# Kernel optimization log

Measured on AMD Instinct MI355X. Metric: run time of the kernel, lower is better.

The kernel has to match this reference:

```python
import jax, jax.numpy as jnp
import numpy as np
import math

B, S, E, H = 2, 1024, 1024, 8
HD = E // H
M, W, K, GH, R, MR = 128, 32, 8, 128, 8, 8
ATTN_ALPHA, GATE_TEMP, CONTENT_MIX = 3.0, 1.0, 0.25
FFN_H = 4 * E


def _layernorm(z, g, b):
    mu = jnp.mean(z, axis=-1, keepdims=True)
    var = jnp.var(z, axis=-1, keepdims=True)
    return (z - mu) * jax.lax.rsqrt(var + 1e-5) * g + b


def _topk_sparse(logits, k, temp):
    # faithful to torch topk_sparse_weights: hard + (soft - hard).detach()
    soft = jax.nn.softmax(logits / max(temp, 1e-6), axis=-1)
    idx = jax.lax.top_k(soft, k)[1]
    hard = jax.nn.one_hot(idx, logits.shape[-1], dtype=soft.dtype).sum(axis=-2)
    hard = hard / (hard.sum(axis=-1, keepdims=True) + 1e-8)
    return hard + jax.lax.stop_gradient(soft - hard)


def _pos_and_window():
    rel = jnp.arange(-(S - 1), S, dtype=jnp.float32)  # [2S-1]
    p1 = rel / S
    p2 = jnp.sign(rel) * jnp.sqrt(jnp.abs(rel) + 1e-6) / math.sqrt(S)
    pos_kern = jnp.stack([p1, p2], axis=-1)  # [2S-1, 2]
    d = jnp.arange(S, dtype=jnp.float32)
    sigma = S / 4.0
    win = jnp.exp(-(d ** 2) / (2.0 * sigma ** 2))  # [S]
    return pos_kern, win


def setup_inputs() -> dict:
    key = jax.random.key(0)
    ks = jax.random.split(key, 20)
    rn = lambda i, shape, s: jax.random.normal(ks[i], shape, dtype=jnp.float32) * s
    scale = 1.0 / math.sqrt(HD)
    return {
        'x': rn(0, (B, S, E), 1.0),
        'v_w': rn(1, (E, E), 0.02), 'v_b': jnp.zeros((E,), jnp.float32),
        'out_w': rn(2, (E, E), 0.02), 'out_b': jnp.zeros((E,), jnp.float32),
        'qmod_w': rn(3, (E, H), 0.02), 'qmod_b': jnp.zeros((H,), jnp.float32),
        'kmod_w': rn(4, (E, H), 0.02), 'kmod_b': jnp.zeros((H,), jnp.float32),
        'gate_w1': rn(5, (H, E, GH), 0.02), 'gate_b1': jnp.zeros((H, GH), jnp.float32),
        'gate_w2': rn(6, (H, GH, M), 0.02), 'gate_b2': jnp.zeros((H, M), jnp.float32),
        'mod_w1': rn(7, (H, E, GH), 0.02), 'mod_b1': jnp.zeros((H, GH), jnp.float32),
        'mod_w2': rn(8, (H, GH, MR), 0.02), 'mod_b2': jnp.zeros((H, MR), jnp.float32),
        'mod_basis': rn(9, (H, MR, M), 0.05),
        'freqs': rn(10, (H, M, W, 2), 1.5),
        'amps': rn(11, (H, M, W), 0.02) + 0.5,
        'phases': rn(12, (H, M, W), math.pi),
        'content_wq': rn(13, (H, HD, R), scale),
        'content_wk': rn(14, (H, HD, R), scale),
        'ffn_w1': rn(15, (E, FFN_H), 0.02), 'ffn_b1': jnp.zeros((FFN_H,), jnp.float32),
        'ffn_w2': rn(16, (FFN_H, E), 0.02), 'ffn_b2': jnp.zeros((E,), jnp.float32),
        'ln_attn_g': jnp.ones((E,), jnp.float32), 'ln_attn_b': jnp.zeros((E,), jnp.float32),
        'ln_ffn_g': jnp.ones((E,), jnp.float32), 'ln_ffn_b': jnp.zeros((E,), jnp.float32),
    }


def reference(x, v_w, v_b, out_w, out_b, qmod_w, qmod_b, kmod_w, kmod_b,
              gate_w1, gate_b1, gate_w2, gate_b2, mod_w1, mod_b1, mod_w2, mod_b2,
              mod_basis, freqs, amps, phases, content_wq, content_wk,
              ffn_w1, ffn_b1, ffn_w2, ffn_b2, ln_attn_g, ln_attn_b, ln_ffn_g, ln_ffn_b):
    pos_kern, win = _pos_and_window()
    # --- per-sequence gating over mask library (top-k sparse routing) ---
    pooled = x.mean(axis=1)  # [B,E]
    gh = jax.nn.relu(jnp.einsum('be,heg->bhg', pooled, gate_w1) + gate_b1)
    glog = jnp.einsum('bhg,hgm->bhm', gh, gate_w2) + gate_b2  # [B,H,M]
    wsel = _topk_sparse(glog, K, GATE_TEMP)
    mh = jax.nn.relu(jnp.einsum('be,heg->bhg', pooled, mod_w1) + mod_b1)
    mr = jnp.einsum('bhg,hgr->bhr', mh, mod_w2) + mod_b2  # [B,H,MR]
    mod = jnp.einsum('bhr,hrm->bhm', mr, mod_basis)
    wmod = wsel * (1.0 + mod)  # [B,H,M]
    # --- wave-interference synthesis of relative-position kernels ---
    dots = jnp.einsum('ld,hmwd->hmwl', pos_kern, freqs)  # [H,M,W,2S-1]
    waves = jnp.sin(2.0 * math.pi * dots + phases[..., None]) * amps[..., None]
    kernels = waves.sum(axis=2)  # [H,M,2S-1]
    kern = jnp.einsum('bhm,hml->bhl', wmod, kernels)  # [B,H,2S-1]
    # --- Toeplitz gather into causal score matrix ---
    i = jnp.arange(S)
    rel_idx = (i[None, :] - i[:, None]) + (S - 1)  # index of rel = j - i
    scores = kern[:, :, rel_idx]  # [B,H,S,S]
    dist = jnp.clip(i[:, None] - i[None, :], 0, S - 1)
    scores = scores * win[dist]
    qs = x @ qmod_w + qmod_b  # [B,S,H]
    km = x @ kmod_w + kmod_b
    logits = ATTN_ALPHA * scores + qs.transpose(0, 2, 1)[..., None] + km.transpose(0, 2, 1)[:, :, None, :]
    # --- low-rank content term ---
    xh = x.reshape(B, S, H, HD)
    qc = jnp.einsum('bshd,hdr->bhsr', xh, content_wq)
    kc = jnp.einsum('bshd,hdr->bhsr', xh, content_wk)
    logits = logits + CONTENT_MIX * jnp.einsum('bhsr,bhtr->bhst', qc, kc)
    causal = i[:, None] >= i[None, :]
    logits = jnp.where(causal, logits, -jnp.inf)
    attn = jax.nn.softmax(logits, axis=-1)
    v = (x @ v_w + v_b).reshape(B, S, H, HD)
    o = jnp.einsum('bhst,bthd->bshd', attn, v).reshape(B, S, E)
    o = o @ out_w + out_b
    y = _layernorm(x + o, ln_attn_g, ln_attn_b)
    f = jax.nn.gelu(y @ ffn_w1 + ffn_b1) @ ffn_w2 + ffn_b2
    return _layernorm(y + f, ln_ffn_g, ln_ffn_b)
```

## Files before the change

### kernel.cpp

```cpp
#include <hip/hip_runtime.h>
#include <math.h>
#include <stdint.h>

namespace {

constexpr int B_ = 2, S_ = 1024, E_ = 1024, H_ = 8, HD_ = 128;
constexpr int M_ = 128, W_ = 32, GH_ = 128, R_ = 8, MR_ = 8, FFNH_ = 4096;
constexpr int SCH = 32;
constexpr int SPC = S_ / SCH;

typedef __bf16 bf16;
typedef _Float16 f16;
typedef __attribute__((ext_vector_type(8))) __bf16 bf16x8;
typedef __attribute__((ext_vector_type(4))) __bf16 bf16x4;
typedef __attribute__((ext_vector_type(4))) _Float16 f16x4;
typedef __attribute__((ext_vector_type(4))) float f32x4;

__device__ inline float gelu_tanh(float u) {
  float u3 = u * u * u;
  return 0.5f * u * (1.f + tanhf(0.7978845608028654f * (u + 0.044715f * u3)));
}

__device__ __forceinline__ void gl_lds16(const void* g, void* l) {
  __builtin_amdgcn_global_load_lds((const __attribute__((address_space(1))) void*)g,
                                   (__attribute__((address_space(3))) void*)l, 16, 0, 0);
}

template <int NB>
__device__ __forceinline__ void gemm_body(
    const bf16* __restrict__ A, const bf16* __restrict__ BT,
    f16* __restrict__ P, int N, int K, int Kslice, size_t strideB, size_t mn,
    int lin, int gx, int gy, bf16* Asb, bf16* Bsb) {
  int t = threadIdx.x;
  int by = lin % gy;
  int rem = lin / gy;
  int bx = rem % gx;
  int z = rem / gx;
  int bb = z % NB;
  int k0 = (z / NB) * Kslice;
  const bf16* Bbase = BT + (size_t)bb * strideB;
  int row0 = by * 128, col0 = bx * 128;
  int lane = t & 63, wid = t >> 6;
  int wr = wid >> 1, wc = wid & 1;

  const bf16* AgP[4];
  const bf16* BgP[4];
  int ldo[4];
#pragma unroll
  for (int j = 0; j < 4; ++j) {
    int p = t + j * 256;
    int sub = p >> 9;
    int pp = p & 511;
    int rt = ((pp >> 6) << 4) | (pp & 15);
    int kb = (pp >> 4) & 3;
    AgP[j] = A + (size_t)(row0 + rt) * K + k0 + sub * 32 + kb * 8;
    BgP[j] = Bbase + (size_t)(col0 + rt) * K + k0 + sub * 32 + kb * 8;
    ldo[j] = sub * 4096 + pp * 8;
  }

  f32x4 acc[4][4];
#pragma unroll
  for (int m = 0; m < 4; ++m)
#pragma unroll
    for (int n = 0; n < 4; ++n) acc[m][n] = (f32x4){0.f, 0.f, 0.f, 0.f};

#pragma unroll
  for (int j = 0; j < 4; ++j) {
    gl_lds16(AgP[j], &Asb[ldo[j]]);
    gl_lds16(BgP[j], &Bsb[ldo[j]]);
  }

  const int nt = Kslice >> 6;
  for (int kt = 0; kt < nt; ++kt) {
    int cur = kt & 1;
    __syncthreads();
    if (kt + 1 < nt) {
      size_t go = (size_t)(kt + 1) * 64;
      int nb = cur ^ 1;
#pragma unroll
      for (int j = 0; j < 4; ++j) {
        gl_lds16(AgP[j] + go, &Asb[nb * 8192 + ldo[j]]);
        gl_lds16(BgP[j] + go, &Bsb[nb * 8192 + ldo[j]]);
      }
    }
#pragma unroll
    for (int kk = 0; kk < 2; ++kk) {
      bf16x8 af[4], bfr[4];
#pragma unroll
      for (int m = 0; m < 4; ++m)
        af[m] = *(const bf16x8*)&Asb[cur * 8192 + kk * 4096 + ((wr * 4 + m) * 64 + lane) * 8];
#pragma unroll
      for (int n = 0; n < 4; ++n)
        bfr[n] = *(const bf16x8*)&Bsb[cur * 8192 + kk * 4096 + ((wc * 4 + n) * 64 + lane) * 8];
#pragma unroll
      for (int m = 0; m < 4; ++m)
#pragma unroll
        for (int n = 0; n < 4; ++n)
          acc[m][n] = __builtin_amdgcn_mfma_f32_16x16x32_bf16(af[m], bfr[n], acc[m][n], 0, 0, 0);
    }
  }

  f16* Pz = P + (size_t)z * mn;
  int r0 = row0 + wr * 64, c0 = col0 + wc * 64;
#pragma unroll
  for (int m = 0; m < 4; ++m)
#pragma unroll
    for (int n = 0; n < 4; ++n) {
      int col = c0 + n * 16 + (lane & 15);
#pragma unroll
      for (int reg = 0; reg < 4; ++reg) {
        int row = r0 + m * 16 + ((lane >> 4) << 2) + reg;
        Pz[(size_t)row * N + col] = (f16)acc[m][n][reg];
      }
    }
}

__device__ __forceinline__ void wt_tile(const float* __restrict__ w,
                                        bf16* __restrict__ wT, int K, int N,
                                        int bx, int by, float (*tile)[33]) {
  int t = threadIdx.x;
  int n0 = bx * 32, k0 = by * 32;
  int tx = t & 31, ty = t >> 5;
  for (int r = ty; r < 32; r += 8) tile[r][tx] = w[(size_t)(k0 + r) * N + n0 + tx];
  __syncthreads();
  for (int r = ty; r < 32; r += 8) wT[(size_t)(n0 + r) * K + k0 + tx] = (bf16)tile[tx][r];
}

__global__ __launch_bounds__(256) void k_prep(
    const float* __restrict__ x, bf16* __restrict__ xb,
    const float* __restrict__ v_w, bf16* __restrict__ vwT,
    const float* __restrict__ qmw, const float* __restrict__ kmw,
    const float* __restrict__ cwq, const float* __restrict__ cwk,
    bf16* __restrict__ wcat, float* __restrict__ part,
    const float* __restrict__ freqs, const float* __restrict__ amps,
    const float* __restrict__ phases, float* __restrict__ kerns) {
  __shared__ float tile[32][33];
  __shared__ float f0[W_], f1[W_], am[W_], ph[W_];
  int b = blockIdx.x, t = threadIdx.x;
  if (b < 2048) {
    size_t i = ((size_t)b * 256 + t) * 4;
    float4 v = *(const float4*)(x + i);
    bf16x4 o;
    o.x = (bf16)v.x; o.y = (bf16)v.y; o.z = (bf16)v.z; o.w = (bf16)v.w;
    *(bf16x4*)(xb + i) = o;
    return;
  }
  if (b < 3072) {
    int l = b - 2048;
    wt_tile(v_w, vwT, 1024, 1024, l & 31, l >> 5, tile);
    return;
  }
  if (b < 4096) {
    int idx = (b - 3072) * 256 + t;
    int n = idx >> 10, k = idx & 1023;
    float v = 0.f;
    if (n < 8) {
      v = qmw[k * 8 + n];
    } else if (n < 16) {
      v = kmw[k * 8 + (n - 8)];
    } else if (n < 80) {
      int u = n - 16, h = u >> 3, r = u & 7;
      int kk = k - h * 128;
      if (kk >= 0 && kk < 128) v = cwq[((size_t)h * 128 + kk) * 8 + r];
    } else if (n < 144) {
      int u = n - 80, h = u >> 3, r = u & 7;
      int kk = k - h * 128;
      if (kk >= 0 && kk < 128) v = cwk[((size_t)h * 128 + kk) * 8 + r];
    }
    wcat[idx] = (bf16)v;
    return;
  }
  if (b < 4160) {
    int b0 = b - 4096;
    int bb = b0 / SCH, c = b0 % SCH;
    const float* xp = x + (size_t)bb * S_ * E_ + (size_t)c * SPC * E_;
    float acc[4] = {0.f, 0.f, 0.f, 0.f};
    for (int s = 0; s < SPC; ++s) {
      const float* row = xp + (size_t)s * E_;
#pragma unroll
      for (int q = 0; q < 4; ++q) acc[q] += row[t + q * 256];
    }
    float* pp = part + (size_t)b0 * E_;
#pragma unroll
    for (int q = 0; q < 4; ++q) pp[t + q * 256] = acc[q];
    return;
  }
  {
    int blk = b - 4160;
    int lt = blk & 3;
    int hm = blk >> 2;
    if (t < W_) {
      f0[t] = freqs[((size_t)hm * W_ + t) * 2 + 0];
      f1[t] = freqs[((size_t)hm * W_ + t) * 2 + 1];
      am[t] = amps[(size_t)hm * W_ + t];
      ph[t] = phases[(size_t)hm * W_ + t];
    }
    __syncthreads();
    int l = lt * 256 + t;
    float rel = (float)(l - (S_ - 1));
    float p1 = rel * (1.0f / S_);
    float p2 = (rel < 0.f) ? (-sqrtf(-rel + 1e-6f) * (1.0f / 32.0f)) : 0.f;
    const float TWO_PI = 6.28318530717958647692f;
    float acc = 0.f;
#pragma unroll
    for (int w = 0; w < W_; ++w)
      acc += am[w] * __sinf(TWO_PI * (f0[w] * p1 + f1[w] * p2) + ph[w]);
    kerns[(size_t)hm * S_ + l] = acc;
  }
}

__global__ __launch_bounds__(256) void k_qv(
    const bf16* __restrict__ xb, const bf16* __restrict__ wcatT,
    f16* __restrict__ Pqk, f16* __restrict__ Pv,
    const bf16* __restrict__ vwT,
    const float* __restrict__ part,
    const float* __restrict__ gw1, const float* __restrict__ mw1,
    float2* __restrict__ gpart) {
  __shared__ bf16 Asb[2 * 8192];
  __shared__ bf16 Bsb[2 * 8192];
  __shared__ float spool[2][64];
  __shared__ float red[2][2][128];
  int b = blockIdx.x, t = threadIdx.x;
  if (b < 256) {
    int lin = (b & 7) * 32 + (b >> 3);
    gemm_body<1>(xb, wcatT, Pqk, 256, E_, 128, 0, (size_t)2048 * 256,
                 lin, 2, 16, Asb, Bsb);
    return;
  }
  if (b >= 512) {
    int l = b - 512;
    int lin = (l & 7) * 64 + (l >> 3);
    gemm_body<2>(vwT, xb, Pv, S_, E_, 256, (size_t)S_ * E_, (size_t)1024 * 1024,
                 lin, 8, 8, Asb, Bsb);
    return;
  }
  int b0 = b - 256;
  int chunk = b0 & 15, h = (b0 >> 4) & 7, mat = b0 >> 7;
  const float* w = mat ? mw1 : gw1;
  if (t < 128) {
    int bb = t >> 6;
    int e = chunk * 64 + (t & 63);
    float s = 0.f;
    for (int c = 0; c < SCH; ++c) s += part[(size_t)(bb * SCH + c) * E_ + e];
    spool[bb][t & 63] = s * (1.0f / S_);
  }
  __syncthreads();
  int g = t & 127, half = t >> 7;
  int e0 = chunk * 64 + half * 32;
  const float* wp = w + (size_t)h * E_ * GH_ + (size_t)e0 * GH_ + g;
  float a0 = 0.f, a1 = 0.f;
#pragma unroll 8
  for (int r = 0; r < 32; ++r) {
    float wv = wp[(size_t)r * GH_];
    a0 += spool[0][half * 32 + r] * wv;
    a1 += spool[1][half * 32 + r] * wv;
  }
  red[half][0][g] = a0;
  red[half][1][g] = a1;
  __syncthreads();
  if (half == 0) {
    float2 o;
    o.x = red[0][0][g] + red[1][0][g];
    o.y = red[0][1][g] + red[1][1][g];
    gpart[(((size_t)mat * H_ + h) * 16 + chunk) * 128 + g] = o;
  }
}

__global__ __launch_bounds__(256) void k_fg2v(
    const f16* __restrict__ Pqk, const float* __restrict__ qmb,
    const float* __restrict__ kmb, float* __restrict__ qsT,
    float* __restrict__ kmT, float* __restrict__ qc, float* __restrict__ kc,
    const float2* __restrict__ gpart,
    const float* __restrict__ gb1, const float* __restrict__ gw2, const float* __restrict__ gb2,
    const float* __restrict__ mb1, const float* __restrict__ mw2, const float* __restrict__ mb2,
    const float* __restrict__ mbasis, float* __restrict__ wmod,
    const f16* __restrict__ Pv, const float* __restrict__ v_b,
    bf16* __restrict__ vT) {
  __shared__ float ghs[GH_], mhs[GH_], glog[M_], mrs[MR_];
  __shared__ float red2[2][128];
  __shared__ float rbuf[128];
  int blk = blockIdx.x, t = threadIdx.x;
  if (blk < 2048) {
    if (t >= 144) return;
    int row = blk;
    int b = row >> 10, s = row & 1023;
    const size_t mn = (size_t)2048 * 256;
    float sum = 0.f;
#pragma unroll
    for (int z = 0; z < 8; ++z) sum += (float)Pqk[(size_t)z * mn + (size_t)row * 256 + t];
    if (t < 8) {
      qsT[((size_t)(b * 8 + t)) * 1024 + s] = sum + qmb[t];
    } else if (t < 16) {
      kmT[((size_t)(b * 8 + t - 8)) * 1024 + s] = sum + kmb[t - 8];
    } else if (t < 80) {
      int u = t - 16, h = u >> 3, r = u & 7;
      qc[(((size_t)(b * 8 + h)) * 1024 + s) * 8 + r] = sum;
    } else {
      int u = t - 80, h = u >> 3, r = u & 7;
      kc[(((size_t)(b * 8 + h)) * 1024 + s) * 8 + r] = sum;
    }
    return;
  }
  if (blk >= 2064) {
    size_t i = ((size_t)(blk - 2064) * 256 + t) * 4;
    const size_t mn = (size_t)1024 * 1024;
    float sx = 0.f, sy = 0.f, sz = 0.f, sw2 = 0.f;
#pragma unroll
    for (int sk = 0; sk < 4; ++sk) {
      f16x4 v = *(const f16x4*)&Pv[(size_t)sk * 2 * mn + i];
      sx += (float)v.x; sy += (float)v.y; sz += (float)v.z; sw2 += (float)v.w;
    }
    float bcol = v_b[(i >> 10) & 1023];
    bf16x4 o;
    o.x = (bf16)(sx + bcol); o.y = (bf16)(sy + bcol);
    o.z = (bf16)(sz + bcol); o.w = (bf16)(sw2 + bcol);
    *(bf16x4*)&vT[i] = o;
    return;
  }
  int bh = blk - 2048;
  int b = bh >> 3, h = bh & 7;
  {
    int g = t & 127, mat = t >> 7;
    const float2* pp = gpart + ((size_t)mat * H_ + h) * 16 * 128 + g;
    float acc = 0.f;
#pragma unroll
    for (int c = 0; c < 16; ++c) {
      float2 v = pp[(size_t)c * 128];
      acc += b ? v.y : v.x;
    }
    acc += (mat ? mb1 : gb1)[h * GH_ + g];
    acc = fmaxf(acc, 0.f);
    if (mat == 0) ghs[g] = acc; else mhs[g] = acc;
  }
  __syncthreads();
  {
    int m = t & 127, half = t >> 7;
    float acc = 0.f;
    const float* wp = gw2 + (size_t)h * GH_ * M_ + m;
#pragma unroll 4
    for (int g = half * 64; g < half * 64 + 64; ++g)
      acc += ghs[g] * wp[(size_t)g * M_];
    red2[half][m] = acc;
  }
  __syncthreads();
  if (t < 128) glog[t] = red2[0][t] + red2[1][t] + gb2[h * M_ + t];
  if (t < 64) {
    int r = t & 7, seg = t >> 3;
    float acc = 0.f;
    const float* wp = mw2 + (size_t)h * GH_ * MR_ + r;
    for (int g = seg * 16; g < seg * 16 + 16; ++g) acc += mhs[g] * wp[(size_t)g * MR_];
    acc += __shfl_xor(acc, 8);
    acc += __shfl_xor(acc, 16);
    acc += __shfl_xor(acc, 32);
    if (t < 8) mrs[t] = acc + mb2[h * MR_ + t];
  }
  __syncthreads();
  if (t < 128) rbuf[t] = glog[t];
  __syncthreads();
  for (int off = 64; off >= 1; off >>= 1) {
    if (t < off) rbuf[t] = fmaxf(rbuf[t], rbuf[t + off]);
    __syncthreads();
  }
  float mx = rbuf[0];
  __syncthreads();
  float ev = 0.f;
  if (t < 128) ev = expf(glog[t] - mx);
  __syncthreads();
  if (t < 128) rbuf[t] = ev;
  __syncthreads();
  for (int off = 64; off >= 1; off >>= 1) {
    if (t < off) rbuf[t] += rbuf[t + off];
    __syncthreads();
  }
  float inv = 1.f / rbuf[0];
  if (t < 128) {
    float wsel = ev * inv;
    float md = 0.f;
#pragma unroll
    for (int r = 0; r < MR_; ++r) md += mrs[r] * mbasis[((size_t)h * MR_ + r) * M_ + t];
    wmod[bh * M_ + t] = wsel * (1.f + md);
  }
}

__global__ __launch_bounds__(256) void k_cs(
    const float* __restrict__ qc, const float* __restrict__ kc,
    bf16* __restrict__ cont,
    const float* __restrict__ wmod, const float* __restrict__ kerns,
    float* __restrict__ swin,
    const float* __restrict__ out_w, bf16* __restrict__ outwT,
    const float* __restrict__ ffn_w1, bf16* __restrict__ ffn1T,
    const float* __restrict__ ffn_w2, bf16* __restrict__ ffn2T) {
  __shared__ float wm[M_];
  __shared__ float tile[32][33];
  int b = blockIdx.x, t = threadIdx.x;
  if (b >= 1088) {
    if (b < 2112) {
      int l = b - 1088;
      wt_tile(out_w, outwT, 1024, 1024, l & 31, l >> 5, tile);
    } else if (b < 6208) {
      int l = b - 2112;
      wt_tile(ffn_w1, ffn1T, 1024, 4096, l & 127, l >> 7, tile);
    } else {
      int l = b - 6208;
      wt_tile(ffn_w2, ffn2T, 4096, 1024, l & 31, l >> 5, tile);
    }
    return;
  }
  int jt = b & 7, it = (b >> 3) & 7, bh = b >> 6;
  if (bh == 16) {
    int blk = it * 8 + jt;
    int dt = blk & 3;
    int sbh = blk >> 2;
    int h = sbh & 7;
    if (t < M_) wm[t] = wmod[sbh * M_ + t];
    __syncthreads();
    int d = dt * 256 + t;
    int l = (S_ - 1) - d;
    float acc = 0.f;
    for (int m = 0; m < M_; ++m) acc += wm[m] * kerns[((size_t)h * M_ + m) * S_ + l];
    float dd = (float)d;
    float win = expf(-dd * dd * (1.0f / 131072.0f));
    swin[(size_t)sbh * S_ + d] = 3.0f * win * acc;
    return;
  }
  if (jt > it) return;
  int w = t >> 6, lane = t & 63;
  int ln = lane & 15, ko = lane >> 4;
  int i0 = it * 128 + w * 32;
  int j0 = jt * 128;

  bf16x8 av[2];
#pragma unroll
  for (int mi = 0; mi < 2; ++mi) {
    bf16x8 a;
#pragma unroll
    for (int k = 0; k < 8; ++k) a[k] = (bf16)0.f;
    if (ko == 0) {
      const float* qp = &qc[((size_t)bh * S_ + i0 + mi * 16 + ln) * 8];
      float4 q0 = *(const float4*)qp;
      float4 q1 = *(const float4*)(qp + 4);
      a[0] = (bf16)q0.x; a[1] = (bf16)q0.y; a[2] = (bf16)q0.z; a[3] = (bf16)q0.w;
      a[4] = (bf16)q1.x; a[5] = (bf16)q1.y; a[6] = (bf16)q1.z; a[7] = (bf16)q1.w;
    }
    av[mi] = a;
  }
  bf16x8 bv[8];
#pragma unroll
  for (int nb = 0; nb < 8; ++nb) {
    bf16x8 bb;
#pragma unroll
    for (int k = 0; k < 8; ++k) bb[k] = (bf16)0.f;
    if (ko == 0) {
      const float* kp = &kc[((size_t)bh * S_ + j0 + nb * 16 + ln) * 8];
      float4 k0 = *(const float4*)kp;
      float4 k1 = *(const float4*)(kp + 4);
      bb[0] = (bf16)k0.x; bb[1] = (bf16)k0.y; bb[2] = (bf16)k0.z; bb[3] = (bf16)k0.w;
      bb[4] = (bf16)k1.x; bb[5] = (bf16)k1.y; bb[6] = (bf16)k1.z; bb[7] = (bf16)k1.w;
    }
    bv[nb] = bb;
  }
  f32x4 acc[2][8];
#pragma unroll
  for (int mi = 0; mi < 2; ++mi)
#pragma unroll
    for (int nb = 0; nb < 8; ++nb) {
      acc[mi][nb] = (f32x4){0.f, 0.f, 0.f, 0.f};
      acc[mi][nb] = __builtin_amdgcn_mfma_f32_16x16x32_bf16(av[mi], bv[nb], acc[mi][nb], 0, 0, 0);
    }
  bf16* cb = cont + ((size_t)bh << 20);
#pragma unroll
  for (int mi = 0; mi < 2; ++mi)
#pragma unroll
    for (int nb = 0; nb < 8; ++nb) {
      int col = j0 + nb * 16 + ln;
#pragma unroll
      for (int reg = 0; reg < 4; ++reg) {
        int row = i0 + mi * 16 + ko * 4 + reg;
        cb[(size_t)row * S_ + col] = (bf16)acc[mi][nb][reg];
      }
    }
}

template <bool GELU, bool RES, bool OUTF32, bool OUTBF16>
__global__ __launch_bounds__(256) void k_gemm_mfma(
    const bf16* __restrict__ A, const bf16* __restrict__ BT,
    const float* __restrict__ bias, const float* __restrict__ res,
    float* __restrict__ C, bf16* __restrict__ Cb, int N, int K) {
  __shared__ bf16 Asb[2][8192];
  __shared__ bf16 Bsb[2][8192];
  int t = threadIdx.x;
  int gx = gridDim.x, gy = gridDim.y;
  int nwg = gx * gy;
  int lin = blockIdx.y * gx + blockIdx.x;
  if (!(nwg & 7)) {
    int cpx = nwg >> 3;
    lin = (lin & 7) * cpx + (lin >> 3);
  }
  int by = lin % gy;
  int bx = lin / gy;
  int row0 = by * 128, col0 = bx * 128;
  int lane = t & 63, wid = t >> 6;
  int wr = wid >> 1, wc = wid & 1;

  const bf16* AgP[4];
  const bf16* BgP[4];
  int ldo[4];
#pragma unroll
  for (int j = 0; j < 4; ++j) {
    int p = t + j * 256;
    int sub = p >> 9;
    int pp = p & 511;
    int rt = ((pp >> 6) << 4) | (pp & 15);
    int kb = (pp >> 4) & 3;
    AgP[j] = A + (size_t)(row0 + rt) * K + sub * 32 + kb * 8;
    BgP[j] = BT + (size_t)(col0 + rt) * K + sub * 32 + kb * 8;
    ldo[j] = sub * 4096 + pp * 8;
  }

  f32x4 acc[4][4];
#pragma unroll
  for (int m = 0; m < 4; ++m)
#pragma unroll
    for (int n = 0; n < 4; ++n) acc[m][n] = (f32x4){0.f, 0.f, 0.f, 0.f};

#pragma unroll
  for (int j = 0; j < 4; ++j) {
    gl_lds16(AgP[j], &Asb[0][ldo[j]]);
    gl_lds16(BgP[j], &Bsb[0][ldo[j]]);
  }

  const int nt = K >> 6;
  for (int kt = 0; kt < nt; ++kt) {
    int cur = kt & 1;
    __syncthreads();
    if (kt + 1 < nt) {
      size_t go = (size_t)(kt + 1) * 64;
      int nb = cur ^ 1;
#pragma unroll
      for (int j = 0; j < 4; ++j) {
        gl_lds16(AgP[j] + go, &Asb[nb][ldo[j]]);
        gl_lds16(BgP[j] + go, &Bsb[nb][ldo[j]]);
      }
    }
#pragma unroll
    for (int kk = 0; kk < 2; ++kk) {
      bf16x8 af[4], bfr[4];
#pragma unroll
      for (int m = 0; m < 4; ++m)
        af[m] = *(const bf16x8*)&Asb[cur][kk * 4096 + ((wr * 4 + m) * 64 + lane) * 8];
#pragma unroll
      for (int n = 0; n < 4; ++n)
        bfr[n] = *(const bf16x8*)&Bsb[cur][kk * 4096 + ((wc * 4 + n) * 64 + lane) * 8];
#pragma unroll
      for (int m = 0; m < 4; ++m)
#pragma unroll
        for (int n = 0; n < 4; ++n)
          acc[m][n] = __builtin_amdgcn_mfma_f32_16x16x32_bf16(af[m], bfr[n], acc[m][n], 0, 0, 0);
    }
  }

  int r0 = row0 + wr * 64, c0 = col0 + wc * 64;
#pragma unroll
  for (int m = 0; m < 4; ++m) {
#pragma unroll
    for (int n = 0; n < 4; ++n) {
      int col = c0 + n * 16 + (lane & 15);
      float bcol = bias[col];
#pragma unroll
      for (int reg = 0; reg < 4; ++reg) {
        int row = r0 + m * 16 + ((lane >> 4) << 2) + reg;
        float u = acc[m][n][reg] + bcol;
        if (GELU) u = gelu_tanh(u);
        if (RES) u += res[(size_t)row * N + col];
        if (OUTF32) C[(size_t)row * N + col] = u;
        if (OUTBF16) Cb[(size_t)row * N + col] = (bf16)u;
      }
    }
  }
}

template <int NB>
__global__ __launch_bounds__(256) void k_gemm_sk(
    const bf16* __restrict__ A, const bf16* __restrict__ BT,
    f16* __restrict__ P, int N, int K, int Kslice, size_t strideB, size_t mn) {
  __shared__ bf16 Asb[2 * 8192];
  __shared__ bf16 Bsb[2 * 8192];
  int gx = gridDim.x, gy = gridDim.y;
  int nwg = gx * gy * gridDim.z;
  int lin = (blockIdx.z * gy + blockIdx.y) * gx + blockIdx.x;
  if (!(nwg & 7)) {
    int cpx = nwg >> 3;
    lin = (lin & 7) * cpx + (lin >> 3);
  }
  gemm_body<NB>(A, BT, P, N, K, Kslice, strideB, mn, lin, gx, gy, Asb, Bsb);
}

template <int SK, bool OUTBF16>
__global__ __launch_bounds__(256) void k_fin_ln(
    const f16* __restrict__ P, const float* __restrict__ bias,
    const float* __restrict__ res, const float* __restrict__ g,
    const float* __restrict__ bb, float* __restrict__ outF,
    bf16* __restrict__ outB) {
  int row = blockIdx.x, t = threadIdx.x;
  size_t base = (size_t)row * E_ + t * 4;
  const size_t mn = (size_t)2048 * 1024;
  float u0 = 0.f, u1 = 0.f, u2 = 0.f, u3 = 0.f;
#pragma unroll
  for (int sk = 0; sk < SK; ++sk) {
    f16x4 v = *(const f16x4*)&P[(size_t)sk * mn + base];
    u0 += (float)v.x; u1 += (float)v.y; u2 += (float)v.z; u3 += (float)v.w;
  }
  float4 bv = *(const float4*)&bias[t * 4];
  float4 rv = *(const float4*)&res[base];
  u0 += bv.x + rv.x; u1 += bv.y + rv.y; u2 += bv.z + rv.z; u3 += bv.w + rv.w;
  float s = u0 + u1 + u2 + u3;
  float s2 = u0 * u0 + u1 * u1 + u2 * u2 + u3 * u3;
#pragma unroll
  for (int off = 32; off >= 1; off >>= 1) {
    s += __shfl_xor(s, off);
    s2 += __shfl_xor(s2, off);
  }
  __shared__ float rs[4], rs2[4];
  int wid = t >> 6;
  if ((t & 63) == 0) { rs[wid] = s; rs2[wid] = s2; }
  __syncthreads();
  float S1 = rs[0] + rs[1] + rs[2] + rs[3];
  float S2 = rs2[0] + rs2[1] + rs2[2] + rs2[3];
  float mu = S1 * (1.f / E_);
  float var = S2 * (1.f / E_) - mu * mu;
  float inv = rsqrtf(var + 1e-5f);
  float4 gv = *(const float4*)&g[t * 4];
  float4 bbv = *(const float4*)&bb[t * 4];
  float4 ov;
  ov.x = (u0 - mu) * inv * gv.x + bbv.x;
  ov.y = (u1 - mu) * inv * gv.y + bbv.y;
  ov.z = (u2 - mu) * inv * gv.z + bbv.z;
  ov.w = (u3 - mu) * inv * gv.w + bbv.w;
  *(float4*)&outF[base] = ov;
  if (OUTBF16) {
    bf16x4 obv;
    obv.x = (bf16)ov.x; obv.y = (bf16)ov.y; obv.z = (bf16)ov.z; obv.w = (bf16)ov.w;
    *(bf16x4*)&outB[base] = obv;
  }
}

__global__ __launch_bounds__(256) void k_attn2(
    const float* __restrict__ qsT, const float* __restrict__ kmT,
    const bf16* __restrict__ cont, const float* __restrict__ swin,
    const bf16* __restrict__ vT,
    bf16* __restrict__ o, bf16* __restrict__ opart, float* __restrict__ mlpart) {
  int q = blockIdx.x & 3;
  int iwg = blockIdx.x >> 2;
  if (q > iwg) return;
  int bh = blockIdx.y;
  int b = bh >> 3, h = bh & 7;
  int t = threadIdx.x;
  int wid = t >> 6, lane = t & 63;
  int iw = iwg * 4 + wid;
  int m = lane & 15, ko = lane >> 4;
  int ntile = iwg + 1;

  __shared__ float sw[S_];
  *(float4*)&sw[t * 4] = *(const float4*)&swin[(size_t)bh * S_ + t * 4];
  __syncthreads();

  int i_row = iw * 16 + m;
  float qs_i = qsT[(size_t)bh * S_ + i_row];
  const bf16* cr = cont + ((size_t)bh << 20) + (size_t)i_row * S_;

  f32x4 acc[8];
#pragma unroll
  for (int nf = 0; nf < 8; ++nf) acc[nf] = (f32x4){0.f, 0.f, 0.f, 0.f};
  float m_run = -INFINITY, l_run = 0.f;

  for (int jt = q; jt < ntile; jt += 4) {
    int j0 = jt * 64;
    float pv[2][8];
    float mx = -INFINITY;
    bf16x8 cv[2];
    cv[0] = *(const bf16x8*)&cr[j0 + ko * 8];
    cv[1] = *(const bf16x8*)&cr[j0 + 32 + ko * 8];
#pragma unroll
    for (int s = 0; s < 2; ++s) {
      int bj = j0 + s * 32 + ko * 8;
      float4 km0 = *(const float4*)&kmT[(size_t)bh * S_ + bj];
      float4 km1 = *(const float4*)&kmT[(size_t)bh * S_ + bj + 4];
      float kmv[8] = {km0.x, km0.y, km0.z, km0.w, km1.x, km1.y, km1.z, km1.w};
#pragma unroll
      for (int e = 0; e < 8; ++e) {
        int j = bj + e;
        int dd = i_row - j;
        float val = sw[dd >= 0 ? dd : 0] + qs_i + kmv[e] + 0.25f * (float)cv[s][e];
        val = (dd >= 0) ? val : -INFINITY;
        pv[s][e] = val;
        mx = fmaxf(mx, val);
      }
    }
    mx = fmaxf(mx, __shfl_xor(mx, 16));
    mx = fmaxf(mx, __shfl_xor(mx, 32));
    float mnew = fmaxf(m_run, mx);
    float scale = __expf(m_run - mnew);
    float lsum = 0.f;
    bf16x8 pa[2];
#pragma unroll
    for (int s = 0; s < 2; ++s)
#pragma unroll
      for (int e = 0; e < 8; ++e) {
        float p = __expf(pv[s][e] - mnew);
        lsum += p;
        pa[s][e] = (bf16)p;
      }
    lsum += __shfl_xor(lsum, 16);
    lsum += __shfl_xor(lsum, 32);
    l_run = l_run * scale + lsum;
    m_run = mnew;
    float sc[4];
#pragma unroll
    for (int r = 0; r < 4; ++r) sc[r] = __shfl(scale, ko * 4 + r);
#pragma unroll
    for (int nf = 0; nf < 8; ++nf)
#pragma unroll
      for (int r = 0; r < 4; ++r) acc[nf][r] *= sc[r];
#pragma unroll
    for (int s = 0; s < 2; ++s) {
      int bj = j0 + s * 32 + ko * 8;
#pragma unroll
      for (int nf = 0; nf < 8; ++nf) {
        int d = nf * 16 + m;
        bf16x8 bv = *(const bf16x8*)&vT[((size_t)bh * HD_ + d) * S_ + bj];
        acc[nf] = __builtin_amdgcn_mfma_f32_16x16x32_bf16(pa[s], bv, acc[nf], 0, 0, 0);
      }
    }
  }

  if (ntile == 1) {
    float lr[4];
#pragma unroll
    for (int r = 0; r < 4; ++r) lr[r] = __shfl(l_run, ko * 4 + r);
#pragma unroll
    for (int nf = 0; nf < 8; ++nf) {
      int d = nf * 16 + m;
#pragma unroll
      for (int r = 0; r < 4; ++r) {
        int row = iw * 16 + ko * 4 + r;
        o[(((size_t)b * S_ + row) * H_ + h) * HD_ + d] = (bf16)(acc[nf][r] / lr[r]);
      }
    }
  } else {
    bf16* op = opart + ((size_t)(q * 16 + bh) * 64 + iw) * 2048;
#pragma unroll
    for (int nf = 0; nf < 8; ++nf) {
      int d = nf * 16 + m;
#pragma unroll
      for (int r = 0; r < 4; ++r) op[(ko * 4 + r) * 128 + d] = (bf16)acc[nf][r];
    }
    if (lane < 16) {
      float* mlp = mlpart + ((size_t)(q * 16 + bh) * 64 + iw) * 32;
      mlp[m * 2 + 0] = m_run;
      mlp[m * 2 + 1] = l_run;
    }
  }
}

__global__ __launch_bounds__(256) void k_comb(const bf16* __restrict__ opart,
                                              const float* __restrict__ mlpart,
                                              bf16* __restrict__ o) {
  int blk = blockIdx.x;
  int bh = blk / 60, iw = blk % 60 + 4;
  int b = bh >> 3, h = bh & 7;
  int t = threadIdx.x;
  int r = t >> 4, d0 = (t & 15) * 8;
  int nq = iw / 4 + 1;
  if (nq > 4) nq = 4;
  float mq[4], lq[4];
  float mm = -INFINITY;
#pragma unroll
  for (int q = 0; q < 4; ++q) {
    if (q < nq) {
      size_t idx = (size_t)(q * 16 + bh) * 64 + iw;
      mq[q] = mlpart[idx * 32 + r * 2];
      lq[q] = mlpart[idx * 32 + r * 2 + 1];
      mm = fmaxf(mm, mq[q]);
    }
  }
  float L = 0.f;
  float acc[8] = {0.f, 0.f, 0.f, 0.f, 0.f, 0.f, 0.f, 0.f};
#pragma unroll
  for (int q = 0; q < 4; ++q) {
    if (q < nq) {
      float e = __expf(mq[q] - mm);
      L += lq[q] * e;
      size_t idx = (size_t)(q * 16 + bh) * 64 + iw;
      bf16x8 v = *(const bf16x8*)&opart[(idx * 16 + r) * 128 + d0];
#pragma unroll
      for (int k = 0; k < 8; ++k) acc[k] += (float)v[k] * e;
    }
  }
  float inv = 1.f / L;
  bf16x8 ov;
#pragma unroll
  for (int k = 0; k < 8; ++k) ov[k] = (bf16)(acc[k] * inv);
  int row = iw * 16 + r;
  *(bf16x8*)&o[(((size_t)b * S_ + row) * H_ + h) * HD_ + d0] = ov;
}

}

extern "C" void kernel_launch(void* const* d_in, const int* in_sizes, int n_in,
                              void* d_out, int out_size, void* d_ws, size_t ws_size,
                              hipStream_t stream) {
  (void)in_sizes; (void)n_in; (void)out_size; (void)ws_size;
  const float* x       = (const float*)d_in[0];
  const float* v_w     = (const float*)d_in[1];
  const float* v_b     = (const float*)d_in[2];
  const float* out_w   = (const float*)d_in[3];
  const float* out_b   = (const float*)d_in[4];
  const float* qmod_w  = (const float*)d_in[5];
  const float* qmod_b  = (const float*)d_in[6];
  const float* kmod_w  = (const float*)d_in[7];
  const float* kmod_b  = (const float*)d_in[8];
  const float* gate_w1 = (const float*)d_in[9];
  const float* gate_b1 = (const float*)d_in[10];
  const float* gate_w2 = (const float*)d_in[11];
  const float* gate_b2 = (const float*)d_in[12];
  const float* mod_w1  = (const float*)d_in[13];
  const float* mod_b1  = (const float*)d_in[14];
  const float* mod_w2  = (const float*)d_in[15];
  const float* mod_b2  = (const float*)d_in[16];
  const float* mod_basis = (const float*)d_in[17];
  const float* freqs   = (const float*)d_in[18];
  const float* amps    = (const float*)d_in[19];
  const float* phases  = (const float*)d_in[20];
  const float* cwq     = (const float*)d_in[21];
  const float* cwk     = (const float*)d_in[22];
  const float* ffn_w1  = (const float*)d_in[23];
  const float* ffn_b1  = (const float*)d_in[24];
  const float* ffn_w2  = (const float*)d_in[25];
  const float* ffn_b2  = (const float*)d_in[26];
  const float* ln_ag   = (const float*)d_in[27];
  const float* ln_ab   = (const float*)d_in[28];
  const float* ln_fg   = (const float*)d_in[29];
  const float* ln_fb   = (const float*)d_in[30];

  char* wsc = (char*)d_ws;
  size_t off = 0;
  auto alloc = [&](size_t bytes) -> void* {
    void* p = wsc + off;
    off += (bytes + 255) & ~(size_t)255;
    return p;
  };
  float* pooled = (float*)alloc(2048 * 4);
  float* part   = (float*)alloc(65536 * 4);
  float2* gpart = (float2*)alloc((size_t)2 * H_ * 16 * 128 * 8);
  float* wmod   = (float*)alloc(2048 * 4);
  float* kerns  = (float*)alloc((size_t)H_ * M_ * S_ * 4);
  float* swin   = (float*)alloc((size_t)B_ * H_ * S_ * 4);
  float* qsT    = (float*)alloc((size_t)B_ * H_ * S_ * 4);
  float* kmT    = (float*)alloc((size_t)B_ * H_ * S_ * 4);
  float* qcb    = (float*)alloc((size_t)B_ * H_ * S_ * R_ * 4);
  float* kcb    = (float*)alloc((size_t)B_ * H_ * S_ * R_ * 4);
  float* ybuf   = (float*)alloc((size_t)B_ * S_ * E_ * 4);
  bf16* xb      = (bf16*)alloc((size_t)B_ * S_ * E_ * 2);
  bf16* yb      = (bf16*)alloc((size_t)B_ * S_ * E_ * 2);
  bf16* vwT     = (bf16*)alloc((size_t)E_ * E_ * 2);
  bf16* outwT   = (bf16*)alloc((size_t)E_ * E_ * 2);
  bf16* ffn1T   = (bf16*)alloc((size_t)E_ * FFNH_ * 2);
  bf16* ffn2T   = (bf16*)alloc((size_t)FFNH_ * E_ * 2);
  bf16* wcatT   = (bf16*)alloc((size_t)256 * E_ * 2);
  bf16* vT      = (bf16*)alloc((size_t)B_ * S_ * E_ * 2);
  bf16* ob      = (bf16*)alloc((size_t)B_ * S_ * E_ * 2);
  float* mlpart = (float*)alloc((size_t)4 * 16 * 64 * 16 * 2 * 4);
  char* poolU2  = (char*)alloc((size_t)B_ * S_ * FFNH_ * 2);
  bf16* opart = (bf16*)poolU2;
  bf16* hb    = (bf16*)poolU2;
  char* P1c = (char*)alloc((size_t)64 * 1024 * 1024);
  f16*  P1  = (f16*)P1c;
  bf16* cont = (bf16*)(P1c + (size_t)16 * 1024 * 1024);
  f16*  P1v  = (f16*)(P1c + (size_t)48 * 1024 * 1024);
  (void)pooled;

  float* outp = (float*)d_out;
  const int BS = B_ * S_;

  k_prep<<<8256, 256, 0, stream>>>(x, xb, v_w, vwT,
                                   qmod_w, kmod_w, cwq, cwk, wcatT,
                                   part, freqs, amps, phases, kerns);

  k_qv<<<1024, 256, 0, stream>>>(xb, wcatT, P1, P1v, vwT,
                                 part, gate_w1, mod_w1, gpart);

  k_fg2v<<<4112, 256, 0, stream>>>(P1, qmod_b, kmod_b, qsT, kmT, qcb, kcb,
                                   gpart, gate_b1, gate_w2, gate_b2,
                                   mod_b1, mod_w2, mod_b2, mod_basis, wmod,
                                   P1v, v_b, vT);

  k_cs<<<10304, 256, 0, stream>>>(qcb, kcb, cont, wmod, kerns, swin,
                                  out_w, outwT, ffn_w1, ffn1T, ffn_w2, ffn2T);

  k_attn2<<<dim3(64, 16), 256, 0, stream>>>(qsT, kmT, cont, swin, vT, ob, opart, mlpart);
  k_comb<<<16 * 60, 256, 0, stream>>>(opart, mlpart, ob);

  k_gemm_sk<1><<<dim3(8, 16, 4), 256, 0, stream>>>(
      ob, outwT, P1, E_, E_, 256, 0, (size_t)2048 * 1024);
  k_fin_ln<4, true><<<2048, 256, 0, stream>>>(P1, out_b, x, ln_ag, ln_ab, ybuf, yb);

  k_gemm_mfma<true, false, false, true><<<dim3(FFNH_ / 128, BS / 128), 256, 0, stream>>>(
      yb, ffn1T, ffn_b1, nullptr, nullptr, hb, FFNH_, E_);

  k_gemm_sk<1><<<dim3(8, 16, 4), 256, 0, stream>>>(
      hb, ffn2T, P1, E_, FFNH_, 1024, 0, (size_t)2048 * 1024);
  k_fin_ln<4, false><<<2048, 256, 0, stream>>>(P1, ffn_b2, ybuf, ln_fg, ln_fb, outp, nullptr);
}
```

Baseline: 222.9 us.

## Replace FFN1 GEMM with 256x256-tile 8-wave pipelined MFMA kernel

Replaces the 128x128-tile, 4-wave FFN1 GEMM (GELU, bf16 output) with a 256x256-tile, 512-thread kernel using 128 KB of dynamic LDS. Each K step is split into half-steps whose global-to-LDS loads are interleaved with MFMA clusters, coordinated by explicit barriers, vmcnt/lgkmcnt waits, sched_barrier and setprio. The aim is more data reuse per tile and better overlap of memory traffic with MFMA work. In exchange, the grid shrinks to 128 workgroups, fewer than the CU count, and the handwritten wait and barrier choreography is fragile.

```diff
diff --git a/kernel.cpp b/kernel.cpp
--- a/kernel.cpp
+++ b/kernel.cpp
@@ -481,13 +481,12 @@
     }
 }
 
-template <bool GELU, bool RES, bool OUTF32, bool OUTBF16>
-__global__ __launch_bounds__(256) void k_gemm_mfma(
+__global__ __launch_bounds__(512, 2) void k_gemm8(
     const bf16* __restrict__ A, const bf16* __restrict__ BT,
-    const float* __restrict__ bias, const float* __restrict__ res,
-    float* __restrict__ C, bf16* __restrict__ Cb, int N, int K) {
-  __shared__ bf16 Asb[2][8192];
-  __shared__ bf16 Bsb[2][8192];
+    const float* __restrict__ bias, bf16* __restrict__ Cb, int N, int K) {
+  extern __shared__ char smem[];
+  char* AsbC = smem;
+  char* BsbC = smem + 65536;
   int t = threadIdx.x;
   int gx = gridDim.x, gy = gridDim.y;
   int nwg = gx * gy;
@@ -498,70 +497,130 @@
   }
   int by = lin % gy;
   int bx = lin / gy;
-  int row0 = by * 128, col0 = bx * 128;
+  int row0 = by * 256, col0 = bx * 256;
   int lane = t & 63, wid = t >> 6;
-  int wr = wid >> 1, wc = wid & 1;
-
-  const bf16* AgP[4];
-  const bf16* BgP[4];
-  int ldo[4];
-#pragma unroll
-  for (int j = 0; j < 4; ++j) {
-    int p = t + j * 256;
-    int sub = p >> 9;
-    int pp = p & 511;
-    int rt = ((pp >> 6) << 4) | (pp & 15);
-    int kb = (pp >> 4) & 3;
-    AgP[j] = A + (size_t)(row0 + rt) * K + sub * 32 + kb * 8;
-    BgP[j] = BT + (size_t)(col0 + rt) * K + sub * 32 + kb * 8;
-    ldo[j] = sub * 4096 + pp * 8;
-  }
-
-  f32x4 acc[4][4];
-#pragma unroll
-  for (int m = 0; m < 4; ++m)
+  int wr = wid >> 2, wc = wid & 3;
+  int fra = wr * 8, frb = wc * 4;
+
+  int s1 = t + 512;
+  int rt0 = ((t >> 6) << 4) | (t & 15);
+  int rt1 = ((s1 >> 6) << 4) | (s1 & 15);
+  int ks0 = ((t >> 4) & 3) << 3;
+  int ks1 = ((s1 >> 4) & 3) << 3;
+  const bf16* Ag0 = A + (size_t)(row0 + rt0) * K + ks0;
+  const bf16* Ag1 = A + (size_t)(row0 + rt1) * K + ks1;
+  const bf16* Bg0 = BT + (size_t)(col0 + rt0) * K + ks0;
+  const bf16* Bg1 = BT + (size_t)(col0 + rt1) * K + ks1;
+  int lo0 = t << 4, lo1 = s1 << 4;
+
+  f32x4 acc[8][4];
+#pragma unroll
+  for (int m = 0; m < 8; ++m)
 #pragma unroll
     for (int n = 0; n < 4; ++n) acc[m][n] = (f32x4){0.f, 0.f, 0.f, 0.f};
 
-#pragma unroll
-  for (int j = 0; j < 4; ++j) {
-    gl_lds16(AgP[j], &Asb[0][ldo[j]]);
-    gl_lds16(BgP[j], &Bsb[0][ldo[j]]);
-  }
-
   const int nt = K >> 6;
+  auto stA = [&](int kt, int kk) {
+    int bo = ((kt & 1) << 15) | (kk << 14);
+    size_t go = (size_t)kt * 64 + (kk << 5);
+    gl_lds16(Ag0 + go, AsbC + bo + lo0);
+    gl_lds16(Ag1 + go, AsbC + bo + lo1);
+  };
+  auto stB = [&](int kt, int kk) {
+    int bo = ((kt & 1) << 15) | (kk << 14);
+    size_t go = (size_t)kt * 64 + (kk << 5);
+    gl_lds16(Bg0 + go, BsbC + bo + lo0);
+    gl_lds16(Bg1 + go, BsbC + bo + lo1);
+  };
+
+  stA(0, 0); stB(0, 0); stA(0, 1); stB(0, 1);
+  if (nt > 1) {
+    stA(1, 0); stB(1, 0);
+    asm volatile("s_waitcnt vmcnt(4)" ::: "memory");
+  } else {
+    asm volatile("s_waitcnt vmcnt(0)" ::: "memory");
+  }
+  __builtin_amdgcn_s_barrier();
+
   for (int kt = 0; kt < nt; ++kt) {
-    int cur = kt & 1;
-    __syncthreads();
+    __builtin_amdgcn_sched_barrier(0);
+    int bo = (kt & 1) << 15;
+    bf16x8 af[4], bfr[4];
+#pragma unroll
+    for (int i = 0; i < 4; ++i)
+      af[i] = *(const bf16x8*)(AsbC + bo + ((fra + i) << 10) + (lane << 4));
+#pragma unroll
+    for (int n = 0; n < 4; ++n)
+      bfr[n] = *(const bf16x8*)(BsbC + bo + ((frb + n) << 10) + (lane << 4));
+    if (kt + 1 < nt) stA(kt + 1, 1);
+    __builtin_amdgcn_s_barrier();
+    asm volatile("s_waitcnt lgkmcnt(0)" ::: "memory");
+    __builtin_amdgcn_sched_barrier(0);
+    __builtin_amdgcn_s_setprio(1);
+#pragma unroll
+    for (int m = 0; m < 4; ++m)
+#pragma unroll
+      for (int n = 0; n < 4; ++n)
+        acc[m][n] = __builtin_amdgcn_mfma_f32_16x16x32_bf16(af[m], bfr[n], acc[m][n], 0, 0, 0);
+    __builtin_amdgcn_s_setprio(0);
+    __builtin_amdgcn_s_barrier();
+#pragma unroll
+    for (int i = 0; i < 4; ++i)
+      af[i] = *(const bf16x8*)(AsbC + bo + ((fra + 4 + i) << 10) + (lane << 4));
+    if (kt + 1 < nt) stB(kt + 1, 1);
+    __builtin_amdgcn_s_barrier();
+    asm volatile("s_waitcnt lgkmcnt(0)" ::: "memory");
+    __builtin_amdgcn_sched_barrier(0);
+    __builtin_amdgcn_s_setprio(1);
+#pragma unroll
+    for (int m = 0; m < 4; ++m)
+#pragma unroll
+      for (int n = 0; n < 4; ++n)
+        acc[4 + m][n] = __builtin_amdgcn_mfma_f32_16x16x32_bf16(af[m], bfr[n], acc[4 + m][n], 0, 0, 0);
+    __builtin_amdgcn_s_setprio(0);
+    __builtin_amdgcn_s_barrier();
+#pragma unroll
+    for (int i = 0; i < 4; ++i)
+      af[i] = *(const bf16x8*)(AsbC + bo + 16384 + ((fra + i) << 10) + (lane << 4));
+#pragma unroll
+    for (int n = 0; n < 4; ++n)
+      bfr[n] = *(const bf16x8*)(BsbC + bo + 16384 + ((frb + n) << 10) + (lane << 4));
+    if (kt + 2 < nt) stA(kt + 2, 0);
+    __builtin_amdgcn_s_barrier();
+    asm volatile("s_waitcnt lgkmcnt(0)" ::: "memory");
+    __builtin_amdgcn_sched_barrier(0);
+    __builtin_amdgcn_s_setprio(1);
+#pragma unroll
+    for (int m = 0; m < 4; ++m)
+#pragma unroll
+      for (int n = 0; n < 4; ++n)
+        acc[m][n] = __builtin_amdgcn_mfma_f32_16x16x32_bf16(af[m], bfr[n], acc[m][n], 0, 0, 0);
+    __builtin_amdgcn_s_setprio(0);
+    __builtin_amdgcn_s_barrier();
+#pragma unroll
+    for (int i = 0; i < 4; ++i)
+      af[i] = *(const bf16x8*)(AsbC + bo + 16384 + ((fra + 4 + i) << 10) + (lane << 4));
+    if (kt + 2 < nt) stB(kt + 2, 0);
+    __builtin_amdgcn_s_barrier();
+    asm volatile("s_waitcnt lgkmcnt(0)" ::: "memory");
+    __builtin_amdgcn_sched_barrier(0);
+    __builtin_amdgcn_s_setprio(1);
+#pragma unroll
+    for (int m = 0; m < 4; ++m)
+#pragma unroll
+      for (int n = 0; n < 4; ++n)
+        acc[4 + m][n] = __builtin_amdgcn_mfma_f32_16x16x32_bf16(af[m], bfr[n], acc[4 + m][n], 0, 0, 0);
+    __builtin_amdgcn_s_setprio(0);
     if (kt + 1 < nt) {
-      size_t go = (size_t)(kt + 1) * 64;
-      int nb = cur ^ 1;
-#pragma unroll
-      for (int j = 0; j < 4; ++j) {
-        gl_lds16(AgP[j] + go, &Asb[nb][ldo[j]]);
-        gl_lds16(BgP[j] + go, &Bsb[nb][ldo[j]]);
-      }
-    }
-#pragma unroll
-    for (int kk = 0; kk < 2; ++kk) {
-      bf16x8 af[4], bfr[4];
-#pragma unroll
-      for (int m = 0; m < 4; ++m)
-        af[m] = *(const bf16x8*)&Asb[cur][kk * 4096 + ((wr * 4 + m) * 64 + lane) * 8];
-#pragma unroll
-      for (int n = 0; n < 4; ++n)
-        bfr[n] = *(const bf16x8*)&Bsb[cur][kk * 4096 + ((wc * 4 + n) * 64 + lane) * 8];
-#pragma unroll
-      for (int m = 0; m < 4; ++m)
-#pragma unroll
-        for (int n = 0; n < 4; ++n)
-          acc[m][n] = __builtin_amdgcn_mfma_f32_16x16x32_bf16(af[m], bfr[n], acc[m][n], 0, 0, 0);
-    }
-  }
-
-  int r0 = row0 + wr * 64, c0 = col0 + wc * 64;
-#pragma unroll
-  for (int m = 0; m < 4; ++m) {
+      if (kt + 2 < nt) asm volatile("s_waitcnt vmcnt(4)" ::: "memory");
+      else             asm volatile("s_waitcnt vmcnt(0)" ::: "memory");
+    }
+    __builtin_amdgcn_s_barrier();
+  }
+
+  int r0 = row0 + wr * 128, c0 = col0 + wc * 64;
+#pragma unroll
+  for (int m = 0; m < 8; ++m)
 #pragma unroll
     for (int n = 0; n < 4; ++n) {
       int col = c0 + n * 16 + (lane & 15);
@@ -569,14 +628,9 @@
 #pragma unroll
       for (int reg = 0; reg < 4; ++reg) {
         int row = r0 + m * 16 + ((lane >> 4) << 2) + reg;
-        float u = acc[m][n][reg] + bcol;
-        if (GELU) u = gelu_tanh(u);
-        if (RES) u += res[(size_t)row * N + col];
-        if (OUTF32) C[(size_t)row * N + col] = u;
-        if (OUTBF16) Cb[(size_t)row * N + col] = (bf16)u;
+        Cb[(size_t)row * N + col] = (bf16)gelu_tanh(acc[m][n][reg] + bcol);
       }
     }
-  }
 }
 
 template <int NB>
@@ -880,7 +934,6 @@
   (void)pooled;
 
   float* outp = (float*)d_out;
-  const int BS = B_ * S_;
 
   k_prep<<<8256, 256, 0, stream>>>(x, xb, v_w, vwT,
                                    qmod_w, kmod_w, cwq, cwk, wcatT,
@@ -904,8 +957,8 @@
       ob, outwT, P1, E_, E_, 256, 0, (size_t)2048 * 1024);
   k_fin_ln<4, true><<<2048, 256, 0, stream>>>(P1, out_b, x, ln_ag, ln_ab, ybuf, yb);
 
-  k_gemm_mfma<true, false, false, true><<<dim3(FFNH_ / 128, BS / 128), 256, 0, stream>>>(
-      yb, ffn1T, ffn_b1, nullptr, nullptr, hb, FFNH_, E_);
+  k_gemm8<<<dim3(FFNH_ / 256, (B_ * S_) / 256), 512, 131072, stream>>>(
+      yb, ffn1T, ffn_b1, hb, FFNH_, E_);
 
   k_gemm_sk<1><<<dim3(8, 16, 4), 256, 0, stream>>>(
       hb, ffn2T, P1, E_, FFNH_, 1024, 0, (size_t)2048 * 1024);
```

After: 231.9 us. +4.0%, slower.
